# Kernel optimization log

Hardware: AMD Instinct MI355X
Metric: run time of the kernel (lower is better)

The kernel has to match this reference:

```python
import jax, jax.numpy as jnp
import numpy as np

T = 4096      # tokens (batch*seq)
D = 1024      # hidden_size
F = 4096      # intermediate_size
E = 8         # num_local_experts


def setup_inputs() -> dict:
    key = jax.random.key(0)
    ks = jax.random.split(key, 6)
    scale_in = 1.0 / np.sqrt(D)
    scale_f = 1.0 / np.sqrt(F)
    return {
        "x": jax.random.normal(ks[0], (T, D), jnp.float32),
        "gate_w": jax.random.normal(ks[1], (E, D), jnp.float32) * scale_in,
        "gate_b": jnp.zeros((E,), jnp.float32),
        "w1": jax.random.normal(ks[2], (E, F, D), jnp.float32) * scale_in,
        "w3": jax.random.normal(ks[3], (E, F, D), jnp.float32) * scale_in,
        "w2": jax.random.normal(ks[4], (E, D, F), jnp.float32) * scale_f,
        "top_k": 2,
    }


def reference(x, gate_w, gate_b, w1, w3, w2, top_k):
    # --- routing: gate linear -> softmax -> top-k, renormalized ---
    logits = x @ gate_w.T + gate_b                     # [T, E]
    probs = jax.nn.softmax(logits, axis=-1)            # [T, E]
    topk_p, topk_i = jax.lax.top_k(probs, top_k)       # [T, k]
    topk_p = topk_p / jnp.sum(topk_p, axis=-1, keepdims=True)
    # dense combine weights [T, E]: zeros except selected experts
    cw = jnp.zeros((x.shape[0], gate_w.shape[0]), x.dtype)
    cw = cw.at[jnp.arange(x.shape[0])[:, None], topk_i].set(topk_p)
    # --- experts: SwiGLU FFN, computed densely per expert, masked combine ---
    h1 = jnp.einsum('td,efd->etf', x, w1)              # [E, T, F]
    h3 = jnp.einsum('td,efd->etf', x, w3)              # [E, T, F]
    act = jax.nn.silu(h1) * h3                         # [E, T, F]
    expert_out = jnp.einsum('etf,edf->etd', act, w2)   # [E, T, D]
    out = jnp.einsum('etd,te->td', expert_out, cw)     # [T, D]
    return out
```

## Files before the change

### kernel.cpp

```cpp
#include <hip/hip_runtime.h>
#include <hip/hip_bf16.h>

#define T_TOK 4096
#define DIM   1024
#define FDIM  4096
#define NEXP  8
#define BM    128
#define BN    128
#define BK    32
#define AM    256
#define AK    32

typedef __attribute__((ext_vector_type(8))) short bf16x8_t;
typedef __attribute__((ext_vector_type(4))) float f32x4_t;

#define GLD16(gp, lp) __builtin_amdgcn_global_load_lds( \
    (const __attribute__((address_space(1))) unsigned int*)(gp), \
    (__attribute__((address_space(3))) unsigned int*)(lp), 16, 0, 0)

__device__ __forceinline__ unsigned short f2bf(float f) {
    union { __hip_bfloat16 h; unsigned short u; } c;
    c.h = __float2bfloat16(f);
    return c.u;
}
__device__ __forceinline__ uint4 pack8(const float4& a, const float4& b) {
    union { unsigned short s[8]; uint4 v; } u;
    u.s[0] = f2bf(a.x); u.s[1] = f2bf(a.y); u.s[2] = f2bf(a.z); u.s[3] = f2bf(a.w);
    u.s[4] = f2bf(b.x); u.s[5] = f2bf(b.y); u.s[6] = f2bf(b.z); u.s[7] = f2bf(b.w);
    return u.v;
}

__global__ __launch_bounds__(256) void convert_kernel(
    const float* __restrict__ src, unsigned short* __restrict__ dst, int n8)
{
    int i = blockIdx.x * 256 + threadIdx.x;
    if (i < n8) {
        const float4* s = reinterpret_cast<const float4*>(src) + (size_t)i * 2;
        float4 a = s[0], b = s[1];
        reinterpret_cast<uint4*>(dst)[i] = pack8(a, b);
    }
}

__global__ __launch_bounds__(256) void gate_kernel(
    const float* __restrict__ x, const float* __restrict__ gw,
    const float* __restrict__ gb, int* __restrict__ cnt,
    int* __restrict__ toklist, float* __restrict__ wlist)
{
    const int lane = threadIdx.x & 63;
    const int wv   = threadIdx.x >> 6;
    const int t    = blockIdx.x * 4 + wv;
    const float* xr = x + (size_t)t * DIM;

    float4 xv[4];
#pragma unroll
    for (int c = 0; c < 4; ++c)
        xv[c] = *reinterpret_cast<const float4*>(xr + c * 256 + lane * 4);

    float logit[NEXP];
#pragma unroll
    for (int e = 0; e < NEXP; ++e) {
        const float* gr = gw + e * DIM;
        float s = 0.f;
#pragma unroll
        for (int c = 0; c < 4; ++c) {
            float4 g = *reinterpret_cast<const float4*>(gr + c * 256 + lane * 4);
            s += xv[c].x * g.x + xv[c].y * g.y + xv[c].z * g.z + xv[c].w * g.w;
        }
#pragma unroll
        for (int o = 32; o > 0; o >>= 1) s += __shfl_xor(s, o, 64);
        logit[e] = s + gb[e];
    }

    if (lane == 0) {
        int i1 = 0;
#pragma unroll
        for (int e = 1; e < NEXP; ++e) if (logit[e] > logit[i1]) i1 = e;
        int i2 = (i1 == 0) ? 1 : 0;
#pragma unroll
        for (int e = 0; e < NEXP; ++e)
            if (e != i1 && e != i2 && logit[e] > logit[i2]) i2 = e;
        float eb = expf(logit[i2] - logit[i1]);
        float wA = 1.f / (1.f + eb);
        float wB = eb / (1.f + eb);
        int p = atomicAdd(&cnt[i1], 1);
        toklist[i1 * T_TOK + p] = t; wlist[i1 * T_TOK + p] = wA;
        p = atomicAdd(&cnt[i2], 1);
        toklist[i2 * T_TOK + p] = t; wlist[i2 * T_TOK + p] = wB;
    }
}

__global__ void offsets_kernel(const int* __restrict__ cnt, int* __restrict__ offs)
{
    if (threadIdx.x == 0) {
        int o = 0;
#pragma unroll
        for (int e = 0; e < NEXP; ++e) {
            offs[e] = o;
            o += ((cnt[e] + AM - 1) / AM) * AM;
        }
    }
}


#define KSTEP(T, PF, VM)                                                       \
  {                                                                            \
    const int buf_ = (T) & 3;                                                  \
    const unsigned short* Ab_  = lds + buf_ * 16384 + wm * 4096 + swz;         \
    const unsigned short* Bb1_ = lds + buf_ * 16384 + 8192 + wnn * 1024 + swz; \
    bf16x8_t af_[8], bf_[2];                                                   \
    _Pragma("unroll")                                                          \
    for (int i_ = 0; i_ < 8; ++i_)                                             \
      af_[i_] = *reinterpret_cast<const bf16x8_t*>(Ab_ + i_ * 512);            \
    bf_[0] = *reinterpret_cast<const bf16x8_t*>(Bb1_);                         \
    bf_[1] = *reinterpret_cast<const bf16x8_t*>(Bb1_ + 512);                   \
    if (PF) {                                                                  \
      const int pb_ = ((T) + 3) & 3;                                           \
      GLD16(Ag0 + ((T) + 3) * AK, lds + pb_ * 16384 + wv * 512);               \
      GLD16(Ag1 + ((T) + 3) * AK, lds + pb_ * 16384 + (wv + 8) * 512);         \
    }                                                                          \
    __builtin_amdgcn_s_barrier();                                              \
    asm volatile("s_waitcnt lgkmcnt(0)" ::: "memory");                         \
    __builtin_amdgcn_sched_barrier(0);                                         \
    __builtin_amdgcn_s_setprio(1);                                             \
    _Pragma("unroll")                                                          \
    for (int j_ = 0; j_ < 2; ++j_)                                             \
      _Pragma("unroll")                                                        \
      for (int i_ = 0; i_ < 8; ++i_)                                           \
        acc1[i_][j_] = __builtin_amdgcn_mfma_f32_16x16x32_bf16(                \
            af_[i_], bf_[j_], acc1[i_][j_], 0, 0, 0);                          \
    __builtin_amdgcn_s_setprio(0);                                             \
    __builtin_amdgcn_s_barrier();                                              \
    bf_[0] = *reinterpret_cast<const bf16x8_t*>(Bb1_ + 4096);                  \
    bf_[1] = *reinterpret_cast<const bf16x8_t*>(Bb1_ + 4096 + 512);            \
    if (PF) {                                                                  \
      const int pb_ = ((T) + 3) & 3;                                           \
      GLD16(B1g + ((T) + 3) * AK, lds + pb_ * 16384 + 8192 + wv * 512);        \
      GLD16(B3g + ((T) + 3) * AK, lds + pb_ * 16384 + 12288 + wv * 512);       \
    }                                                                          \
    asm volatile("s_waitcnt " VM ::: "memory");                                \
    __builtin_amdgcn_s_barrier();                                              \
    asm volatile("s_waitcnt lgkmcnt(0)" ::: "memory");                         \
    __builtin_amdgcn_sched_barrier(0);                                         \
    __builtin_amdgcn_s_setprio(1);                                             \
    _Pragma("unroll")                                                          \
    for (int j_ = 0; j_ < 2; ++j_)                                             \
      _Pragma("unroll")                                                        \
      for (int i_ = 0; i_ < 8; ++i_)                                           \
        acc3[i_][j_] = __builtin_amdgcn_mfma_f32_16x16x32_bf16(                \
            af_[i_], bf_[j_], acc3[i_][j_], 0, 0, 0);                          \
    __builtin_amdgcn_s_setprio(0);                                             \
    __builtin_amdgcn_s_barrier();                                              \
  }

__global__ __launch_bounds__(512, 2) void stageA_kernel(
    const unsigned short* __restrict__ xb, const unsigned short* __restrict__ w1b,
    const unsigned short* __restrict__ w3b, const int* __restrict__ cnt,
    const int* __restrict__ offs, const int* __restrict__ toklist,
    const unsigned short* __restrict__ zbuf, unsigned short* __restrict__ act)
{
    const int e  = blockIdx.z;
    const int c  = cnt[e];
    const int mt = blockIdx.y;
    if (mt * AM >= c) return;
    const int nt = blockIdx.x;
    const int n0 = nt * 128;

    __shared__ __align__(16) unsigned short lds[4 * 16384];

    const int tid  = threadIdx.x;
    const int lane = tid & 63;
    const int wv   = tid >> 6;
    const int wm   = wv >> 2;
    const int wnn  = wv & 3;
    const int quad = lane >> 4;
    const int r    = lane & 15;

    const int swz = (r * 32 + quad * 8) ^ (((r >> 1) & 3) << 3);

    const int wr = (lane >> 2) & 15;
    const int wc = (((lane ^ (lane >> 3)) & 1) << 3) |
                   ((((lane >> 1) ^ (lane >> 4)) & 1) << 4);

    const int stRow = wv * 16 + wr;
    const int ar0 = mt * AM + stRow;
    const int ar1 = ar0 + 128;
    const unsigned short* Ag0 = (ar0 < c)
        ? xb + (size_t)toklist[e * T_TOK + ar0] * DIM + wc : zbuf + wc;
    const unsigned short* Ag1 = (ar1 < c)
        ? xb + (size_t)toklist[e * T_TOK + ar1] * DIM + wc : zbuf + wc;
    const unsigned short* B1g = w1b + ((size_t)e * FDIM + n0 + stRow) * DIM + wc;
    const unsigned short* B3g = w3b + ((size_t)e * FDIM + n0 + stRow) * DIM + wc;

    f32x4_t acc1[8][2], acc3[8][2];
#pragma unroll
    for (int i = 0; i < 8; ++i)
#pragma unroll
        for (int j = 0; j < 2; ++j) {
            acc1[i][j] = (f32x4_t){0.f, 0.f, 0.f, 0.f};
            acc3[i][j] = (f32x4_t){0.f, 0.f, 0.f, 0.f};
        }

#pragma unroll
    for (int t = 0; t < 3; ++t) {
        GLD16(Ag0 + t * AK, lds + t * 16384 + wv * 512);
        GLD16(Ag1 + t * AK, lds + t * 16384 + (wv + 8) * 512);
        GLD16(B1g + t * AK, lds + t * 16384 + 8192 + wv * 512);
        GLD16(B3g + t * AK, lds + t * 16384 + 12288 + wv * 512);
    }
    asm volatile("s_waitcnt vmcnt(8)" ::: "memory");
    __builtin_amdgcn_s_barrier();

#pragma unroll 1
    for (int t = 0; t < 28; ++t) KSTEP(t, 1, "vmcnt(8)");
    KSTEP(28, 1, "vmcnt(8)");
    KSTEP(29, 0, "vmcnt(4)");
    KSTEP(30, 0, "vmcnt(0)");
    KSTEP(31, 0, "vmcnt(0)");

    const size_t slot0 = (size_t)offs[e] + (size_t)mt * AM;
    unsigned short* abase = act + (slot0 + wm * 128 + quad * 4) * (size_t)FDIM
                          + n0 + wnn * 32 + r;
#pragma unroll
    for (int i = 0; i < 8; ++i)
#pragma unroll
        for (int j = 0; j < 2; ++j)
#pragma unroll
            for (int rr = 0; rr < 4; ++rr) {
                float h1 = acc1[i][j][rr];
                float h3 = acc3[i][j][rr];
                float sw = h1 / (1.f + __expf(-h1)) * h3;
                abase[(size_t)(i * 16 + rr) * FDIM + j * 16] = f2bf(sw);
            }
}

__global__ __launch_bounds__(256, 3) void stageB_kernel(
    const unsigned short* __restrict__ act, const unsigned short* __restrict__ w2b,
    const int* __restrict__ cnt, const int* __restrict__ offs,
    const int* __restrict__ toklist, const float* __restrict__ wlist,
    float* __restrict__ out)
{
    const int e  = blockIdx.z & 7;
    const int ks = blockIdx.z >> 3;
    const int c  = cnt[e];
    const int mt = blockIdx.y;
    if (mt * BM >= c) return;
    const int nt = blockIdx.x;
    const size_t slot0 = (size_t)offs[e] + (size_t)mt * BM;
    const int n0 = nt * BN;
    const int kbase = ks * (FDIM / 2);

    __shared__ __align__(16) unsigned short As[BM * BK];
    __shared__ __align__(16) unsigned short Bs[BN * BK];

    const int tid  = threadIdx.x;
    const int lane = tid & 63;
    const int wv   = tid >> 6;
    const int wm   = (wv & 1) * 64;
    const int wn   = (wv >> 1) * 64;
    const int quad = lane >> 4;
    const int r    = lane & 15;

    const int dRow = wv * 32 + (lane >> 2);
    const unsigned short* Adma = act + (slot0 + dRow) * FDIM + kbase + (lane & 3) * 8;
    const unsigned short* Bdma = w2b + ((size_t)e * DIM + n0 + dRow) * FDIM + kbase + (lane & 3) * 8;
    const int lds0 = (wv * 32) * BK;
    const int lds1 = (wv * 32 + 16) * BK;

    f32x4_t acc[4][4];
#pragma unroll
    for (int i = 0; i < 4; ++i)
#pragma unroll
        for (int j = 0; j < 4; ++j) acc[i][j] = (f32x4_t){0.f, 0.f, 0.f, 0.f};

    for (int kd = 0; kd < FDIM / 2; kd += BK) {
        __syncthreads();
        GLD16(Adma + kd,             &As[lds0]);
        GLD16(Adma + kd + 16 * FDIM, &As[lds1]);
        GLD16(Bdma + kd,             &Bs[lds0]);
        GLD16(Bdma + kd + 16 * FDIM, &Bs[lds1]);
        __syncthreads();

        bf16x8_t af[4];
#pragma unroll
        for (int i = 0; i < 4; ++i)
            af[i] = *reinterpret_cast<const bf16x8_t*>(&As[(wm + i * 16 + r) * BK + quad * 8]);
#pragma unroll
        for (int j = 0; j < 4; ++j) {
            bf16x8_t bf = *reinterpret_cast<const bf16x8_t*>(&Bs[(wn + j * 16 + r) * BK + quad * 8]);
#pragma unroll
            for (int i = 0; i < 4; ++i)
                acc[i][j] = __builtin_amdgcn_mfma_f32_16x16x32_bf16(af[i], bf, acc[i][j], 0, 0, 0);
        }
    }

    const int row0 = mt * BM;
#pragma unroll
    for (int i = 0; i < 4; ++i)
#pragma unroll
        for (int rr = 0; rr < 4; ++rr) {
            int m = wm + i * 16 + quad * 4 + rr;
            int row = row0 + m;
            if (row < c) {
                int tok  = toklist[e * T_TOK + row];
                float wt = wlist[e * T_TOK + row];
                float* orow = out + (size_t)tok * DIM + n0;
#pragma unroll
                for (int j = 0; j < 4; ++j) {
                    int n = wn + j * 16 + r;
                    atomicAdd(&orow[n], wt * acc[i][j][rr]);
                }
            }
        }
}

extern "C" void kernel_launch(void* const* d_in, const int* in_sizes, int n_in,
                              void* d_out, int out_size, void* d_ws, size_t ws_size,
                              hipStream_t stream)
{
    (void)in_sizes; (void)n_in; (void)out_size; (void)ws_size;
    const float* x  = (const float*)d_in[0];
    const float* gw = (const float*)d_in[1];
    const float* gb = (const float*)d_in[2];
    const float* w1 = (const float*)d_in[3];
    const float* w3 = (const float*)d_in[4];
    const float* w2 = (const float*)d_in[5];
    float* out = (float*)d_out;

    char* ws = (char*)d_ws;
    unsigned short* xb   = (unsigned short*)ws;
    unsigned short* act  = (unsigned short*)(ws + 8388608);
    unsigned short* w1b  = (unsigned short*)(ws + 92274688);
    unsigned short* w3b  = (unsigned short*)(ws + 159383552);
    unsigned short* w2b  = (unsigned short*)(ws + 226492416);
    unsigned short* zbuf = (unsigned short*)(ws + 293601280);
    int*   cnt     = (int*)(ws + 293605376);
    int*   offs    = cnt + 64;
    int*   toklist = cnt + 128;
    float* wlist   = (float*)(cnt + 128 + NEXP * T_TOK);

    hipMemsetAsync(cnt, 0, 64, stream);
    hipMemsetAsync(zbuf, 0, 4096, stream);
    hipMemsetAsync(out, 0, (size_t)T_TOK * DIM * sizeof(float), stream);

    const int n8 = NEXP * FDIM * DIM / 8;
    convert_kernel<<<n8 / 256, 256, 0, stream>>>(w1, w1b, n8);
    convert_kernel<<<n8 / 256, 256, 0, stream>>>(w3, w3b, n8);
    convert_kernel<<<n8 / 256, 256, 0, stream>>>(w2, w2b, n8);
    convert_kernel<<<(T_TOK * DIM / 8) / 256, 256, 0, stream>>>(x, xb, T_TOK * DIM / 8);

    gate_kernel<<<T_TOK / 4, 256, 0, stream>>>(x, gw, gb, cnt, toklist, wlist);
    offsets_kernel<<<1, 64, 0, stream>>>(cnt, offs);
    stageA_kernel<<<dim3(FDIM / 128, T_TOK / AM, NEXP), 512, 0, stream>>>(
        xb, w1b, w3b, cnt, offs, toklist, zbuf, act);
    stageB_kernel<<<dim3(DIM / BN, T_TOK / BM, NEXP * 2), 256, 0, stream>>>(
        act, w2b, cnt, offs, toklist, wlist, out);
}
```

Baseline: 825.5 us.

## Register double-buffer A fragments and merge stage-A k-step into one barrier phase

```diff
diff --git a/kernel.cpp b/kernel.cpp
--- a/kernel.cpp
+++ b/kernel.cpp
@@ -102,53 +102,37 @@
 }
 
 
-#define KSTEP(T, PF, VM)                                                       \
+#define ASTEP(TC, AFC, AFN, PF, RDNEXT, VM)                                    \
   {                                                                            \
-    const int buf_ = (T) & 3;                                                  \
-    const unsigned short* Ab_  = lds + buf_ * 16384 + wm * 4096 + swz;         \
-    const unsigned short* Bb1_ = lds + buf_ * 16384 + 8192 + wnn * 1024 + swz; \
-    bf16x8_t af_[8], bf_[2];                                                   \
-    _Pragma("unroll")                                                          \
-    for (int i_ = 0; i_ < 8; ++i_)                                             \
-      af_[i_] = *reinterpret_cast<const bf16x8_t*>(Ab_ + i_ * 512);            \
-    bf_[0] = *reinterpret_cast<const bf16x8_t*>(Bb1_);                         \
-    bf_[1] = *reinterpret_cast<const bf16x8_t*>(Bb1_ + 512);                   \
+    const unsigned short* bufc_ = lds + ((TC) & 3) * 16384;                    \
+    bf16x8_t b1a_ = *reinterpret_cast<const bf16x8_t*>(bufc_ + 8192  + wnn * 1024 + swz);       \
+    bf16x8_t b1b_ = *reinterpret_cast<const bf16x8_t*>(bufc_ + 8192  + wnn * 1024 + 512 + swz); \
+    bf16x8_t b3a_ = *reinterpret_cast<const bf16x8_t*>(bufc_ + 12288 + wnn * 1024 + swz);       \
+    bf16x8_t b3b_ = *reinterpret_cast<const bf16x8_t*>(bufc_ + 12288 + wnn * 1024 + 512 + swz); \
+    if (RDNEXT) {                                                              \
+      const unsigned short* bufn_ = lds + (((TC) + 1) & 3) * 16384 + wm * 4096 + swz; \
+      _Pragma("unroll")                                                        \
+      for (int i_ = 0; i_ < 8; ++i_)                                           \
+        AFN[i_] = *reinterpret_cast<const bf16x8_t*>(bufn_ + i_ * 512);        \
+    }                                                                          \
+    __builtin_amdgcn_sched_barrier(0);                                         \
     if (PF) {                                                                  \
-      const int pb_ = ((T) + 3) & 3;                                           \
-      GLD16(Ag0 + ((T) + 3) * AK, lds + pb_ * 16384 + wv * 512);               \
-      GLD16(Ag1 + ((T) + 3) * AK, lds + pb_ * 16384 + (wv + 8) * 512);         \
+      const int pb_ = ((TC) + 3) & 3;                                          \
+      GLD16(Ag0 + ((TC) + 3) * AK, lds + pb_ * 16384 + wv * 512);              \
+      GLD16(Ag1 + ((TC) + 3) * AK, lds + pb_ * 16384 + (wv + 8) * 512);        \
+      GLD16(B1g + ((TC) + 3) * AK, lds + pb_ * 16384 + 8192 + wv * 512);       \
+      GLD16(B3g + ((TC) + 3) * AK, lds + pb_ * 16384 + 12288 + wv * 512);      \
     }                                                                          \
-    __builtin_amdgcn_s_barrier();                                              \
-    asm volatile("s_waitcnt lgkmcnt(0)" ::: "memory");                         \
-    __builtin_amdgcn_sched_barrier(0);                                         \
     __builtin_amdgcn_s_setprio(1);                                             \
     _Pragma("unroll")                                                          \
-    for (int j_ = 0; j_ < 2; ++j_)                                             \
-      _Pragma("unroll")                                                        \
-      for (int i_ = 0; i_ < 8; ++i_)                                           \
-        acc1[i_][j_] = __builtin_amdgcn_mfma_f32_16x16x32_bf16(                \
-            af_[i_], bf_[j_], acc1[i_][j_], 0, 0, 0);                          \
+    for (int i_ = 0; i_ < 8; ++i_) {                                           \
+      acc1[i_][0] = __builtin_amdgcn_mfma_f32_16x16x32_bf16(AFC[i_], b1a_, acc1[i_][0], 0, 0, 0); \
+      acc1[i_][1] = __builtin_amdgcn_mfma_f32_16x16x32_bf16(AFC[i_], b1b_, acc1[i_][1], 0, 0, 0); \
+      acc3[i_][0] = __builtin_amdgcn_mfma_f32_16x16x32_bf16(AFC[i_], b3a_, acc3[i_][0], 0, 0, 0); \
+      acc3[i_][1] = __builtin_amdgcn_mfma_f32_16x16x32_bf16(AFC[i_], b3b_, acc3[i_][1], 0, 0, 0); \
+    }                                                                          \
     __builtin_amdgcn_s_setprio(0);                                             \
-    __builtin_amdgcn_s_barrier();                                              \
-    bf_[0] = *reinterpret_cast<const bf16x8_t*>(Bb1_ + 4096);                  \
-    bf_[1] = *reinterpret_cast<const bf16x8_t*>(Bb1_ + 4096 + 512);            \
-    if (PF) {                                                                  \
-      const int pb_ = ((T) + 3) & 3;                                           \
-      GLD16(B1g + ((T) + 3) * AK, lds + pb_ * 16384 + 8192 + wv * 512);        \
-      GLD16(B3g + ((T) + 3) * AK, lds + pb_ * 16384 + 12288 + wv * 512);       \
-    }                                                                          \
     asm volatile("s_waitcnt " VM ::: "memory");                                \
-    __builtin_amdgcn_s_barrier();                                              \
-    asm volatile("s_waitcnt lgkmcnt(0)" ::: "memory");                         \
-    __builtin_amdgcn_sched_barrier(0);                                         \
-    __builtin_amdgcn_s_setprio(1);                                             \
-    _Pragma("unroll")                                                          \
-    for (int j_ = 0; j_ < 2; ++j_)                                             \
-      _Pragma("unroll")                                                        \
-      for (int i_ = 0; i_ < 8; ++i_)                                           \
-        acc3[i_][j_] = __builtin_amdgcn_mfma_f32_16x16x32_bf16(                \
-            af_[i_], bf_[j_], acc3[i_][j_], 0, 0, 0);                          \
-    __builtin_amdgcn_s_setprio(0);                                             \
     __builtin_amdgcn_s_barrier();                                              \
   }
 
@@ -207,15 +191,26 @@
         GLD16(B1g + t * AK, lds + t * 16384 + 8192 + wv * 512);
         GLD16(B3g + t * AK, lds + t * 16384 + 12288 + wv * 512);
     }
-    asm volatile("s_waitcnt vmcnt(8)" ::: "memory");
+    asm volatile("s_waitcnt vmcnt(4)" ::: "memory");
     __builtin_amdgcn_s_barrier();
 
+    bf16x8_t afA[8], afB[8];
+    {
+        const unsigned short* b0 = lds + wm * 4096 + swz;
+#pragma unroll
+        for (int i = 0; i < 8; ++i)
+            afA[i] = *reinterpret_cast<const bf16x8_t*>(b0 + i * 512);
+    }
+
 #pragma unroll 1
-    for (int t = 0; t < 28; ++t) KSTEP(t, 1, "vmcnt(8)");
-    KSTEP(28, 1, "vmcnt(8)");
-    KSTEP(29, 0, "vmcnt(4)");
-    KSTEP(30, 0, "vmcnt(0)");
-    KSTEP(31, 0, "vmcnt(0)");
+    for (int t = 0; t < 28; t += 2) {
+        ASTEP(t,     afA, afB, 1, 1, "vmcnt(4)");
+        ASTEP(t + 1, afB, afA, 1, 1, "vmcnt(4)");
+    }
+    ASTEP(28, afA, afB, 1, 1, "vmcnt(4)");
+    ASTEP(29, afB, afA, 0, 1, "vmcnt(0)");
+    ASTEP(30, afA, afB, 0, 1, "vmcnt(0)");
+    ASTEP(31, afB, afA, 0, 0, "vmcnt(0)");
 
     const size_t slot0 = (size_t)offs[e] + (size_t)mt * AM;
     unsigned short* abase = act + (slot0 + wm * 128 + quad * 4) * (size_t)FDIM
```

Result: no change. 822.7 us (-0.3%).
